# Optimization experiments

Hardware: AMD Instinct MI355X
Metric: run time of the kernel (lower is better)

The kernel has to match this reference:

```python
import jax, jax.numpy as jnp
import numpy as np

EMB = 64
HID = 1024
SEQ = 9
BATCH = 4096


def setup_inputs() -> dict:
    key = jax.random.key(0)
    ks = jax.random.split(key, 10)
    s = lambda *sh: 1.0 / np.sqrt(sh[-1])
    return {
        "observed": jax.random.normal(ks[0], (SEQ, BATCH, 2), dtype=jnp.float32),
        "W_emb": jax.random.normal(ks[1], (EMB, 2), dtype=jnp.float32) * s(2),
        "b_emb": jnp.zeros((EMB,), dtype=jnp.float32),
        "W_ih": jax.random.normal(ks[2], (4 * HID, EMB), dtype=jnp.float32) * s(EMB),
        "b_ih": jnp.zeros((4 * HID,), dtype=jnp.float32),
        "W_hh": jax.random.normal(ks[3], (4 * HID, HID), dtype=jnp.float32) * s(HID),
        "b_hh": jnp.zeros((4 * HID,), dtype=jnp.float32),
        "W_out": jax.random.normal(ks[4], (5, HID), dtype=jnp.float32) * s(HID),
        "b_out": jnp.zeros((5,), dtype=jnp.float32),
        "n_predict": 12,
    }


def _cell(x, h, c, W_ih, b_ih, W_hh, b_hh):
    # torch.nn.LSTMCell gate math, gate order i, f, g, o
    gates = x @ W_ih.T + b_ih + h @ W_hh.T + b_hh  # [B, 4H]
    i, f, g, o = jnp.split(gates, 4, axis=-1)
    c_new = jax.nn.sigmoid(f) * c + jax.nn.sigmoid(i) * jnp.tanh(g)
    h_new = jax.nn.sigmoid(o) * jnp.tanh(c_new)
    return h_new, c_new


def reference(observed, W_emb, b_emb, W_ih, b_ih, W_hh, b_hh, W_out, b_out, n_predict):
    B = observed.shape[1]
    H = W_hh.shape[1]
    h0 = jnp.zeros((B, H), dtype=observed.dtype)
    c0 = jnp.zeros((B, H), dtype=observed.dtype)

    diffs = observed[1:] - observed[:-1]  # [SEQ-1, B, 2]

    def obs_step(carry, d):
        h, c = carry
        emb = jax.nn.relu(d @ W_emb.T + b_emb)  # [B, EMB]
        h, c = _cell(emb, h, c, W_ih, b_ih, W_hh, b_hh)
        normal = h @ W_out.T + b_out  # [B, 5]
        return (h, c), normal

    (h, c), normals_obs = jax.lax.scan(obs_step, (h0, c0), diffs)
    new_vel = normals_obs[-1][:, :2]

    def pred_step(carry, _):
        h, c, nv = carry
        emb = jax.nn.relu(jax.lax.stop_gradient(nv) @ W_emb.T + b_emb)
        h, c = _cell(emb, h, c, W_ih, b_ih, W_hh, b_hh)
        normal = h @ W_out.T + b_out
        return (h, c, normal[:, :2]), normal

    (_, _, _), normals_pred = jax.lax.scan(
        pred_step, (h, c, new_vel), None, length=n_predict - 1)

    # training-mode output: stacked raw 'normal' params, shape [SEQ-1+n_predict-1, B, 5]
    return jnp.concatenate([normals_obs, normals_pred], axis=0)
```

## Files before the change

kernel.cpp:

```cpp
#include <hip/hip_runtime.h>
#include <stdint.h>
#include <stddef.h>

#define BATCH 4096
#define HID   1024
#define EMB   64
#define KDIM  1088
#define NKT   34
#define NSTEP 19
#define NOBS  8

typedef _Float16 f16;
typedef _Float16 half8 __attribute__((ext_vector_type(8)));
typedef float    float4v __attribute__((ext_vector_type(4)));

__device__ __forceinline__ float sigm(float x) { return 1.f / (1.f + __expf(-x)); }
__device__ __forceinline__ float tanh_f(float x) { return 1.f - 2.f / (__expf(2.f * x) + 1.f); }

__device__ __forceinline__ int xf_idx(int row, int k) {
  return ((((row >> 4) * NKT + (k >> 5)) * 64) + (row & 15) + (((k >> 3) & 3) << 4)) * 8 + (k & 7);
}

__global__ void pack_kernel(const float* __restrict__ W_ih, const float* __restrict__ b_ih,
                            const float* __restrict__ W_hh, const float* __restrict__ b_hh,
                            f16* __restrict__ Wsw, float* __restrict__ bc) {
  int gid = blockIdx.x * blockDim.x + threadIdx.x;
  int j = gid & 7;
  int lane = (gid >> 3) & 63;
  int c16 = (gid >> 9) & 255;
  int kt = gid >> 17;
  int p = c16 * 16 + (lane & 15);
  int k = kt * 32 + ((lane >> 4) << 3) + j;
  int t = p >> 7, g = (p >> 5) & 3, u = p & 31;
  int orig = g * HID + t * 32 + u;
  float val = (k < EMB) ? W_ih[orig * EMB + k] : W_hh[orig * HID + (k - EMB)];
  Wsw[gid] = (f16)val;
  if (k == 0) bc[p] = b_ih[orig] + b_hh[orig];
}

__global__ void emb0_kernel(const float* __restrict__ observed,
                            const float* __restrict__ W_emb, const float* __restrict__ b_emb,
                            f16* __restrict__ Xf) {
  int gid = blockIdx.x * blockDim.x + threadIdx.x;
  int b = gid >> 6, j = gid & 63;
  const float* o0 = observed + b * 2;
  const float* o1 = o0 + BATCH * 2;
  float d0 = o1[0] - o0[0];
  float d1 = o1[1] - o0[1];
  float v = d0 * W_emb[2 * j] + d1 * W_emb[2 * j + 1] + b_emb[j];
  Xf[xf_idx(b, j)] = (f16)fmaxf(v, 0.f);
}

__global__ __launch_bounds__(256, 2)
void gemm_cell_kernel(const f16* __restrict__ Xf, const f16* __restrict__ Wsw,
                      const float* __restrict__ bc,
                      float* __restrict__ c_ws, f16* __restrict__ Xn,
                      const float* __restrict__ obs_next, int do_emb,
                      const float* __restrict__ W_emb, const float* __restrict__ b_emb) {
  const int tid = threadIdx.x;
  const int lane = tid & 63;
  const int w = tid >> 6;
  const int l15 = lane & 15;
  const int quad = lane >> 4;
  const int tt = blockIdx.x;
  const int mB = blockIdx.y;
  const int rt0 = mB * 16 + w * 4;

  const f16* aB = Xf + (size_t)rt0 * (NKT * 512) + lane * 8;
  const f16* bB = Wsw + (size_t)tt * 8 * 512 + lane * 8;

  float4v acc[4][8];
#pragma unroll
  for (int mi = 0; mi < 4; ++mi)
#pragma unroll
    for (int ni = 0; ni < 8; ++ni) acc[mi][ni] = (float4v){0.f, 0.f, 0.f, 0.f};

  half8 afA[4], bfA[8], afB[4], bfB[8];

#define LOADF(af, bf, kt)                                                          \
  do {                                                                             \
    _Pragma("unroll") for (int mi = 0; mi < 4; ++mi)                               \
        af[mi] = *(const half8*)(aB + mi * (NKT * 512) + (kt) * 512);              \
    _Pragma("unroll") for (int ni = 0; ni < 8; ++ni)                               \
        bf[ni] = *(const half8*)(bB + ni * 512 + (kt) * 131072);                   \
  } while (0)

#define MFMA_ALL(af, bf)                                                           \
  do {                                                                             \
    _Pragma("unroll") for (int mi = 0; mi < 4; ++mi)                               \
    _Pragma("unroll") for (int ni = 0; ni < 8; ++ni)                               \
        acc[mi][ni] =                                                              \
            __builtin_amdgcn_mfma_f32_16x16x32_f16(af[mi], bf[ni], acc[mi][ni], 0, 0, 0); \
  } while (0)

  LOADF(afA, bfA, 0);
  for (int i = 0; i < NKT / 2; ++i) {
    const int k1 = 2 * i + 1;
    LOADF(afB, bfB, k1);
    MFMA_ALL(afA, bfA);
    if (k1 + 1 < NKT) LOADF(afA, bfA, k1 + 1);
    MFMA_ALL(afB, bfB);
  }
#undef LOADF
#undef MFMA_ALL

  float bias[8];
#pragma unroll
  for (int ni = 0; ni < 8; ++ni) bias[ni] = bc[tt * 128 + ni * 16 + l15];

  float* cbase = c_ws + ((size_t)(mB * 32 + tt) * 256 + tid) * 32;
  float4v cv[8];
#pragma unroll
  for (int q = 0; q < 8; ++q) cv[q] = *(const float4v*)(cbase + q * 4);

#pragma unroll
  for (int mi = 0; mi < 4; ++mi) {
#pragma unroll
    for (int u16 = 0; u16 < 2; ++u16) {
      const int j = tt * 32 + u16 * 16 + l15;
      const int ci = mi * 2 + u16;
#pragma unroll
      for (int r = 0; r < 4; ++r) {
        const int row = mB * 256 + w * 64 + mi * 16 + quad * 4 + r;
        float gi = acc[mi][u16 + 0][r] + bias[u16 + 0];
        float gf = acc[mi][u16 + 2][r] + bias[u16 + 2];
        float gg = acc[mi][u16 + 4][r] + bias[u16 + 4];
        float go = acc[mi][u16 + 6][r] + bias[u16 + 6];
        float cn = sigm(gf) * cv[ci][r] + sigm(gi) * tanh_f(gg);
        cv[ci][r] = cn;
        float h = sigm(go) * tanh_f(cn);
        Xn[xf_idx(row, EMB + j)] = (f16)h;
      }
    }
  }
#pragma unroll
  for (int q = 0; q < 8; ++q) *(float4v*)(cbase + q * 4) = cv[q];

  if (do_emb && tt == 0) {
    const int row = mB * 256 + tid;
    const float* o0 = obs_next + row * 2;
    const float* o1 = o0 + BATCH * 2;
    float d0 = o1[0] - o0[0];
    float d1 = o1[1] - o0[1];
#pragma unroll
    for (int j = 0; j < EMB; ++j) {
      float v = d0 * W_emb[2 * j] + d1 * W_emb[2 * j + 1] + b_emb[j];
      Xn[xf_idx(row, j)] = (f16)fmaxf(v, 0.f);
    }
  }
}

__global__ __launch_bounds__(256)
void outemb_kernel(const f16* __restrict__ Xh, const float* __restrict__ W_out,
                   const float* __restrict__ b_out, float* __restrict__ out_t,
                   int emb_flag, const float* __restrict__ W_emb,
                   const float* __restrict__ b_emb, f16* __restrict__ Xn) {
  __shared__ float red[4][16][5];
  __shared__ float s_nv[16][2];
  const int tid = threadIdx.x;
  const int lane = tid & 63;
  const int w = tid >> 6;
  const int l15 = lane & 15;
  const int quad = lane >> 4;
  const int rt = blockIdx.x;

  float a[5] = {0.f, 0.f, 0.f, 0.f, 0.f};
#pragma unroll
  for (int i = 0; i < 8; ++i) {
    const int kt = 2 + w + 4 * i;
    half8 hv = *(const half8*)(Xh + ((rt * NKT + kt) * 64 + lane) * 8);
    const float* wo = W_out + kt * 32 + quad * 8 - EMB;
#pragma unroll
    for (int o = 0; o < 5; ++o) {
      const float* wp = wo + o * HID;
      float s = 0.f;
#pragma unroll
      for (int e = 0; e < 8; ++e) s += (float)hv[e] * wp[e];
      a[o] += s;
    }
  }
#pragma unroll
  for (int o = 0; o < 5; ++o) {
    a[o] += __shfl_xor(a[o], 16, 64);
    a[o] += __shfl_xor(a[o], 32, 64);
  }
  if (quad == 0)
#pragma unroll
    for (int o = 0; o < 5; ++o) red[w][l15][o] = a[o];
  __syncthreads();
  if (tid < 80) {
    const int row = tid / 5, o = tid - row * 5;
    float v = red[0][row][o] + red[1][row][o] + red[2][row][o] + red[3][row][o] + b_out[o];
    out_t[(size_t)(rt * 16 + row) * 5 + o] = v;
    if (o < 2) s_nv[row][o] = v;
  }
  if (emb_flag) {
    __syncthreads();
    for (int s = tid; s < 1024; s += 256) {
      const int rr = s >> 6, jc = s & 63;
      const int row = rt * 16 + rr;
      float d0 = s_nv[rr][0], d1 = s_nv[rr][1];
      float v = d0 * W_emb[2 * jc] + d1 * W_emb[2 * jc + 1] + b_emb[jc];
      Xn[xf_idx(row, jc)] = (f16)fmaxf(v, 0.f);
    }
  }
}

extern "C" void kernel_launch(void* const* d_in, const int* in_sizes, int n_in,
                              void* d_out, int out_size, void* d_ws, size_t ws_size,
                              hipStream_t stream) {
  const float* observed = (const float*)d_in[0];
  const float* W_emb = (const float*)d_in[1];
  const float* b_emb = (const float*)d_in[2];
  const float* W_ih = (const float*)d_in[3];
  const float* b_ih = (const float*)d_in[4];
  const float* W_hh = (const float*)d_in[5];
  const float* b_hh = (const float*)d_in[6];
  const float* W_out = (const float*)d_in[7];
  const float* b_out = (const float*)d_in[8];
  float* out = (float*)d_out;

  uint8_t* ws = (uint8_t*)d_ws;
  const size_t WC_BYTES = (size_t)4096 * KDIM * sizeof(f16);
  f16* Wsw = (f16*)ws;
  float* bc = (float*)(ws + WC_BYTES);
  f16* X0 = (f16*)(ws + WC_BYTES + 16384);
  f16* X1 = (f16*)(ws + 2 * WC_BYTES + 16384);
  float* c_ws = (float*)(ws + 3 * WC_BYTES + 16384);

  pack_kernel<<<(4096 * KDIM) / 256, 256, 0, stream>>>(W_ih, b_ih, W_hh, b_hh, Wsw, bc);
  hipMemsetAsync(X0, 0, WC_BYTES, stream);
  hipMemsetAsync(c_ws, 0, (size_t)BATCH * HID * 4, stream);
  emb0_kernel<<<(BATCH * EMB) / 256, 256, 0, stream>>>(observed, W_emb, b_emb, X0);

  for (int t = 0; t < NSTEP; ++t) {
    f16* Xc = (t & 1) ? X1 : X0;
    f16* Xn = (t & 1) ? X0 : X1;
    const int do_emb = (t + 1 < NOBS) ? 1 : 0;
    dim3 grid(32, 16);
    gemm_cell_kernel<<<grid, 256, 0, stream>>>(
        Xc, Wsw, bc, c_ws, Xn, observed + (size_t)(t + 1) * BATCH * 2, do_emb, W_emb, b_emb);
    const int emb_pred = (t >= 7 && t + 1 < NSTEP) ? 1 : 0;
    outemb_kernel<<<BATCH / 16, 256, 0, stream>>>(
        Xn, W_out, b_out, out + (size_t)t * BATCH * 5, emb_pred, W_emb, b_emb, Xn);
  }
}
```

Baseline: 1.100 ms.

## Fuse output projection into LSTM cell epilogue and store cell state in fp16

The GEMM cell epilogue now computes per-tile partial dot products of h with W_out, reduces them across lanes with shuffles, and writes them to a partials buffer. A light reduce kernel sums the 32 column-tile partials, adds the bias and does the prediction embedding. This replaces the old kernel that re-read all of h. The cell state is also stored in fp16 instead of fp32, halving its traffic but adding rounding error that accumulates across 19 recurrent steps. The embedding writes are vectorized into half8 stores.

```diff
diff --git a/kernel.cpp b/kernel.cpp
--- a/kernel.cpp
+++ b/kernel.cpp
@@ -54,7 +54,8 @@
 __global__ __launch_bounds__(256, 2)
 void gemm_cell_kernel(const f16* __restrict__ Xf, const f16* __restrict__ Wsw,
                       const float* __restrict__ bc,
-                      float* __restrict__ c_ws, f16* __restrict__ Xn,
+                      f16* __restrict__ c_ws, f16* __restrict__ Xn,
+                      float* __restrict__ po_ws, const float* __restrict__ W_out,
                       const float* __restrict__ obs_next, int do_emb,
                       const float* __restrict__ W_emb, const float* __restrict__ b_emb) {
   const int tid = threadIdx.x;
@@ -108,33 +109,56 @@
 #pragma unroll
   for (int ni = 0; ni < 8; ++ni) bias[ni] = bc[tt * 128 + ni * 16 + l15];
 
-  float* cbase = c_ws + ((size_t)(mB * 32 + tt) * 256 + tid) * 32;
-  float4v cv[8];
-#pragma unroll
-  for (int q = 0; q < 8; ++q) cv[q] = *(const float4v*)(cbase + q * 4);
+  float wb[2][5];
+#pragma unroll
+  for (int u16 = 0; u16 < 2; ++u16)
+#pragma unroll
+    for (int o = 0; o < 5; ++o)
+      wb[u16][o] = W_out[o * HID + tt * 32 + u16 * 16 + l15];
+
+  f16* cbase = c_ws + ((size_t)(mB * 32 + tt) * 256 + tid) * 32;
+  half8 cv8[4];
+#pragma unroll
+  for (int q = 0; q < 4; ++q) cv8[q] = *(const half8*)(cbase + q * 8);
 
 #pragma unroll
   for (int mi = 0; mi < 4; ++mi) {
 #pragma unroll
-    for (int u16 = 0; u16 < 2; ++u16) {
-      const int j = tt * 32 + u16 * 16 + l15;
-      const int ci = mi * 2 + u16;
-#pragma unroll
-      for (int r = 0; r < 4; ++r) {
-        const int row = mB * 256 + w * 64 + mi * 16 + quad * 4 + r;
+    for (int r = 0; r < 4; ++r) {
+      const int row = mB * 256 + w * 64 + mi * 16 + quad * 4 + r;
+      float pa[5] = {0.f, 0.f, 0.f, 0.f, 0.f};
+#pragma unroll
+      for (int u16 = 0; u16 < 2; ++u16) {
+        const int j = tt * 32 + u16 * 16 + l15;
+        const int ce = (mi * 2 + u16) * 4 + r;
         float gi = acc[mi][u16 + 0][r] + bias[u16 + 0];
         float gf = acc[mi][u16 + 2][r] + bias[u16 + 2];
         float gg = acc[mi][u16 + 4][r] + bias[u16 + 4];
         float go = acc[mi][u16 + 6][r] + bias[u16 + 6];
-        float cn = sigm(gf) * cv[ci][r] + sigm(gi) * tanh_f(gg);
-        cv[ci][r] = cn;
+        float co = (float)cv8[ce >> 3][ce & 7];
+        float cn = sigm(gf) * co + sigm(gi) * tanh_f(gg);
+        cv8[ce >> 3][ce & 7] = (f16)cn;
         float h = sigm(go) * tanh_f(cn);
         Xn[xf_idx(row, EMB + j)] = (f16)h;
+#pragma unroll
+        for (int o = 0; o < 5; ++o) pa[o] += h * wb[u16][o];
+      }
+#pragma unroll
+      for (int o = 0; o < 5; ++o) {
+        pa[o] += __shfl_xor(pa[o], 1, 64);
+        pa[o] += __shfl_xor(pa[o], 2, 64);
+        pa[o] += __shfl_xor(pa[o], 4, 64);
+        pa[o] += __shfl_xor(pa[o], 8, 64);
+      }
+      if (l15 == 0) {
+        float* pdst = po_ws + ((size_t)tt * BATCH + row) * 5;
+#pragma unroll
+        for (int o = 0; o < 5; ++o) pdst[o] = pa[o];
       }
     }
   }
 #pragma unroll
-  for (int q = 0; q < 8; ++q) *(float4v*)(cbase + q * 4) = cv[q];
+  for (int q = 0; q < 4; ++q) *(half8*)(cbase + q * 8) = cv8[q];
 
   if (do_emb && tt == 0) {
     const int row = mB * 256 + tid;
@@ -142,67 +166,55 @@
     const float* o1 = o0 + BATCH * 2;
     float d0 = o1[0] - o0[0];
     float d1 = o1[1] - o0[1];
-#pragma unroll
-    for (int j = 0; j < EMB; ++j) {
-      float v = d0 * W_emb[2 * j] + d1 * W_emb[2 * j + 1] + b_emb[j];
-      Xn[xf_idx(row, j)] = (f16)fmaxf(v, 0.f);
-    }
+    const int rt = row >> 4;
+#pragma unroll
+    for (int kt = 0; kt < 2; ++kt)
+#pragma unroll
+      for (int kl = 0; kl < 4; ++kl) {
+        half8 hv;
+#pragma unroll
+        for (int e = 0; e < 8; ++e) {
+          int j = kt * 32 + kl * 8 + e;
+          float v = d0 * W_emb[2 * j] + d1 * W_emb[2 * j + 1] + b_emb[j];
+          hv[e] = (f16)fmaxf(v, 0.f);
+        }
+        *(half8*)(Xn + (((rt * NKT + kt) * 64) + (row & 15) + 16 * kl) * 8) = hv;
+      }
   }
 }
 
 __global__ __launch_bounds__(256)
-void outemb_kernel(const f16* __restrict__ Xh, const float* __restrict__ W_out,
-                   const float* __restrict__ b_out, float* __restrict__ out_t,
-                   int emb_flag, const float* __restrict__ W_emb,
-                   const float* __restrict__ b_emb, f16* __restrict__ Xn) {
-  __shared__ float red[4][16][5];
-  __shared__ float s_nv[16][2];
+void reduce_kernel(const float* __restrict__ po_ws, const float* __restrict__ b_out,
+                   float* __restrict__ out_t, int emb_flag,
+                   const float* __restrict__ W_emb, const float* __restrict__ b_emb,
+                   f16* __restrict__ Xn) {
+  __shared__ float s_nv[32][2];
   const int tid = threadIdx.x;
-  const int lane = tid & 63;
-  const int w = tid >> 6;
-  const int l15 = lane & 15;
-  const int quad = lane >> 4;
-  const int rt = blockIdx.x;
-
-  float a[5] = {0.f, 0.f, 0.f, 0.f, 0.f};
-#pragma unroll
-  for (int i = 0; i < 8; ++i) {
-    const int kt = 2 + w + 4 * i;
-    half8 hv = *(const half8*)(Xh + ((rt * NKT + kt) * 64 + lane) * 8);
-    const float* wo = W_out + kt * 32 + quad * 8 - EMB;
-#pragma unroll
-    for (int o = 0; o < 5; ++o) {
-      const float* wp = wo + o * HID;
-      float s = 0.f;
-#pragma unroll
-      for (int e = 0; e < 8; ++e) s += (float)hv[e] * wp[e];
-      a[o] += s;
-    }
-  }
-#pragma unroll
-  for (int o = 0; o < 5; ++o) {
-    a[o] += __shfl_xor(a[o], 16, 64);
-    a[o] += __shfl_xor(a[o], 32, 64);
-  }
-  if (quad == 0)
-#pragma unroll
-    for (int o = 0; o < 5; ++o) red[w][l15][o] = a[o];
-  __syncthreads();
-  if (tid < 80) {
-    const int row = tid / 5, o = tid - row * 5;
-    float v = red[0][row][o] + red[1][row][o] + red[2][row][o] + red[3][row][o] + b_out[o];
-    out_t[(size_t)(rt * 16 + row) * 5 + o] = v;
-    if (o < 2) s_nv[row][o] = v;
+  const int r0 = blockIdx.x * 32;
+
+  if (tid < 160) {
+    const int rowl = tid / 5, o = tid - rowl * 5;
+    const int row = r0 + rowl;
+    float s = 0.f;
+#pragma unroll
+    for (int tt = 0; tt < 32; ++tt) s += po_ws[((size_t)tt * BATCH + row) * 5 + o];
+    float v = s + b_out[o];
+    out_t[(size_t)row * 5 + o] = v;
+    if (o < 2) s_nv[rowl][o] = v;
   }
   if (emb_flag) {
     __syncthreads();
-    for (int s = tid; s < 1024; s += 256) {
-      const int rr = s >> 6, jc = s & 63;
-      const int row = rt * 16 + rr;
-      float d0 = s_nv[rr][0], d1 = s_nv[rr][1];
-      float v = d0 * W_emb[2 * jc] + d1 * W_emb[2 * jc + 1] + b_emb[jc];
-      Xn[xf_idx(row, jc)] = (f16)fmaxf(v, 0.f);
+    const int rowl = tid >> 3, kt = (tid >> 2) & 1, kl = tid & 3;
+    const int row = r0 + rowl;
+    const float d0 = s_nv[rowl][0], d1 = s_nv[rowl][1];
+    half8 hv;
+#pragma unroll
+    for (int e = 0; e < 8; ++e) {
+      int j = kt * 32 + kl * 8 + e;
+      float v = d0 * W_emb[2 * j] + d1 * W_emb[2 * j + 1] + b_emb[j];
+      hv[e] = (f16)fmaxf(v, 0.f);
     }
+    *(half8*)(Xn + ((((row >> 4) * NKT + kt) * 64) + (row & 15) + 16 * kl) * 8) = hv;
   }
 }
 
@@ -226,11 +238,12 @@
   float* bc = (float*)(ws + WC_BYTES);
   f16* X0 = (f16*)(ws + WC_BYTES + 16384);
   f16* X1 = (f16*)(ws + 2 * WC_BYTES + 16384);
-  float* c_ws = (float*)(ws + 3 * WC_BYTES + 16384);
+  f16* c_ws = (f16*)(ws + 3 * WC_BYTES + 16384);
+  float* po_ws = (float*)(ws + 3 * WC_BYTES + 16384 + (size_t)BATCH * HID * 2);
 
   pack_kernel<<<(4096 * KDIM) / 256, 256, 0, stream>>>(W_ih, b_ih, W_hh, b_hh, Wsw, bc);
   hipMemsetAsync(X0, 0, WC_BYTES, stream);
-  hipMemsetAsync(c_ws, 0, (size_t)BATCH * HID * 4, stream);
+  hipMemsetAsync(c_ws, 0, (size_t)BATCH * HID * 2, stream);
   emb0_kernel<<<(BATCH * EMB) / 256, 256, 0, stream>>>(observed, W_emb, b_emb, X0);
 
   for (int t = 0; t < NSTEP; ++t) {
@@ -239,9 +252,10 @@
     const int do_emb = (t + 1 < NOBS) ? 1 : 0;
     dim3 grid(32, 16);
     gemm_cell_kernel<<<grid, 256, 0, stream>>>(
-        Xc, Wsw, bc, c_ws, Xn, observed + (size_t)(t + 1) * BATCH * 2, do_emb, W_emb, b_emb);
+        Xc, Wsw, bc, c_ws, Xn, po_ws, W_out,
+        observed + (size_t)(t + 1) * BATCH * 2, do_emb, W_emb, b_emb);
     const int emb_pred = (t >= 7 && t + 1 < NSTEP) ? 1 : 0;
-    outemb_kernel<<<BATCH / 16, 256, 0, stream>>>(
-        Xn, W_out, b_out, out + (size_t)t * BATCH * 5, emb_pred, W_emb, b_emb, Xn);
-  }
-}
+    reduce_kernel<<<BATCH / 32, 256, 0, stream>>>(
+        po_ws, b_out, out + (size_t)t * BATCH * 5, emb_pred, W_emb, b_emb, Xn);
+  }
+}
```

Result: slower. 1.145 ms (+4.1%).
